# Kernel optimization log

Hardware: AMD Instinct MI355X
Metric: run time of the kernel (lower is better)

## Reference

```python
import jax, jax.numpy as jnp
import numpy as np

# Static problem constants (must match setup_inputs)
NUM_GRAPHS = 64      # batch_size = int(batch[-1]) + 1
PTS_PER_GRAPH = 512
RATIO = 16           # centroids per graph
HEADS = 4
IN_CH = 64           # = out_channels per head (concat=False -> mean over heads)
NEG_SLOPE = 0.2


def setup_inputs() -> dict:
    key = jax.random.key(0)
    ks = jax.random.split(key, 8)
    N = NUM_GRAPHS * PTS_PER_GRAPH
    x = jax.random.normal(ks[0], (N, IN_CH), dtype=jnp.float32)
    edge_index = jnp.zeros((2, 2), dtype=jnp.int64)  # unused by forward
    batch = (jnp.arange(N) // PTS_PER_GRAPH).astype(jnp.int64)
    xcent_base = jax.random.normal(ks[1], (RATIO, IN_CH), dtype=jnp.float32)
    W_l = jax.random.normal(ks[2], (IN_CH, HEADS * IN_CH), dtype=jnp.float32) / np.sqrt(IN_CH)
    b_l = jax.random.normal(ks[3], (HEADS * IN_CH,), dtype=jnp.float32) * 0.01
    W_r = jax.random.normal(ks[4], (IN_CH, HEADS * IN_CH), dtype=jnp.float32) / np.sqrt(IN_CH)
    b_r = jax.random.normal(ks[5], (HEADS * IN_CH,), dtype=jnp.float32) * 0.01
    att = jax.random.normal(ks[6], (HEADS, IN_CH), dtype=jnp.float32) / np.sqrt(IN_CH)
    bias = jax.random.normal(ks[7], (IN_CH,), dtype=jnp.float32) * 0.01
    return {"x": x, "edge_index": edge_index, "batch": batch,
            "xcent_base": xcent_base, "W_l": W_l, "b_l": b_l,
            "W_r": W_r, "b_r": b_r, "att": att, "bias": bias}


def _bipart_pool(x, batch, xcent_base, W_l, b_l, W_r, b_r, att, bias):
    N = x.shape[0]
    B = NUM_GRAPHS
    Nc = B * RATIO  # number of centroid (target) nodes

    # Dense bipartite edges: each source node -> all RATIO centroids of its graph.
    src = jnp.repeat(jnp.arange(N, dtype=jnp.int32), RATIO)                     # [E]
    dst = jnp.tile(jnp.arange(RATIO, dtype=jnp.int32), N) \
        + jnp.repeat(batch.astype(jnp.int32), RATIO) * RATIO                    # [E]

    # PyG GATv2Conv(add_self_loops=True): remove src==dst edges, then add
    # self loops (i,i) for i < min(N_src, N_dst) = Nc. Keep static shapes by
    # masking the removed edges instead of deleting them.
    self_idx = jnp.arange(Nc, dtype=jnp.int32)
    src_f = jnp.concatenate([src, self_idx])
    dst_f = jnp.concatenate([dst, self_idx])
    drop = jnp.concatenate([src == dst, jnp.zeros((Nc,), dtype=bool)])          # [E+Nc]

    # Linear projections (source and target sides)
    x_l = (x @ W_l + b_l).reshape(N, HEADS, IN_CH)                              # [N,H,C]
    xcent = jnp.tile(xcent_base, (B, 1))                                        # [Nc,IN]
    x_r = (xcent @ W_r + b_r).reshape(Nc, HEADS, IN_CH)                         # [Nc,H,C]

    # GATv2 attention: leaky_relu(x_i + x_j) . att, softmax per target node
    xj = x_l[src_f]                                                             # [E',H,C]
    g = jax.nn.leaky_relu(xj + x_r[dst_f], NEG_SLOPE)
    alpha = jnp.einsum('ehc,hc->eh', g, att)                                    # [E',H]
    alpha = jnp.where(drop[:, None], jnp.float32(-1e30), alpha)
    amax = jax.ops.segment_max(alpha, dst_f, num_segments=Nc)                   # [Nc,H]
    e = jnp.exp(alpha - amax[dst_f])
    den = jax.ops.segment_sum(e, dst_f, num_segments=Nc)                        # [Nc,H]
    w = e / den[dst_f]                                                          # [E',H]

    out = jax.ops.segment_sum(w[..., None] * xj, dst_f, num_segments=Nc)        # [Nc,H,C]
    out = out.mean(axis=1) + bias                                               # concat=False -> mean heads
    return out.reshape(B, RATIO, IN_CH)


def reference(x, edge_index, batch, xcent_base, W_l, b_l, W_r, b_r, att, bias):
    xcent = _bipart_pool(x, batch, xcent_base, W_l, b_l, W_r, b_r, att, bias)
    batchcent = jnp.repeat(jnp.arange(NUM_GRAPHS, dtype=jnp.int64), RATIO)
    return xcent, batchcent
```

## Files before the change

kernel.cpp:

```cpp
#include <hip/hip_runtime.h>

#define PTS 512
#define CH  64
#define NC  1024

using s8v = __attribute__((ext_vector_type(8))) short;
using f4v = __attribute__((ext_vector_type(4))) float;

static __device__ __forceinline__ unsigned short f2b(float f) {
    unsigned u = __float_as_uint(f);
    return (unsigned short)((u + 0x7FFFu + ((u >> 16) & 1u)) >> 16);
}
static __device__ __forceinline__ float b2f(unsigned short s) {
    return __uint_as_float((unsigned)s << 16);
}

__global__ __launch_bounds__(256) void k0(
    const float* __restrict__ xcb, const float* __restrict__ W_r,
    const float* __restrict__ b_r, const float* __restrict__ att,
    float* __restrict__ axr, float* __restrict__ sxr)
{
    __shared__ float s_row[256];
    const int h = blockIdx.x >> 2, rq = blockIdx.x & 3;
    const int rl = threadIdx.x >> 6, c = threadIdx.x & 63;
    const int r = rq * 4 + rl;
    float acc = b_r[h * 64 + c];
    for (int k = 0; k < 64; ++k)
        acc = fmaf(xcb[r * 64 + k], W_r[k * 256 + h * 64 + c], acc);
    axr[(h * 16 + r) * 64 + c] = fabsf(att[h * 64 + c]) * acc;
    s_row[rl * 64 + c] = acc;
    __syncthreads();
    if (threadIdx.x < 4) {
        float s = 0.f;
        for (int cc = 0; cc < 64; ++cc)
            s = fmaf(s_row[threadIdx.x * 64 + cc], att[h * 64 + cc], s);
        sxr[h * 16 + rq * 4 + threadIdx.x] = s;
    }
}

__global__ __launch_bounds__(256, 2) void k1(
    const float* __restrict__ x, const float* __restrict__ W_l,
    const float* __restrict__ b_l, const float* __restrict__ att,
    const float* __restrict__ axr_ws, const float* __restrict__ sxr_ws,
    const float* __restrict__ bias,
    float* __restrict__ aws, unsigned short* __restrict__ xlself,
    float* __restrict__ out)
{
    __shared__ unsigned short s_xl[64 * 264];
    __shared__ float s_axr[4096];
    __shared__ float s_patt[256], s_sgn[256];
    __shared__ float s_sxr[64];

    const int tid = threadIdx.x;
    const int lane = tid & 63;
    const int w = __builtin_amdgcn_readfirstlane(tid >> 6);
    const int blk = blockIdx.x;
    const int row0 = blk * 64;
    const int l15 = lane & 15, quad = lane >> 4;

    {
        float av = att[tid];
        s_patt[tid] = fabsf(av);
        s_sgn[tid] = av < 0.f ? -1.f : 1.f;
    }
    for (int idx = tid; idx < 4096; idx += 256) s_axr[idx] = axr_ws[idx];
    if (tid < 64) s_sxr[tid] = sxr_ws[tid];

    f4v acc[4][4];
    const f4v zf = {0.f, 0.f, 0.f, 0.f};
#pragma unroll
    for (int m = 0; m < 4; ++m)
#pragma unroll
        for (int n = 0; n < 4; ++n) acc[m][n] = zf;

#pragma unroll
    for (int ks = 0; ks < 2; ++ks) {
        s8v Af[4], Bf[4];
#pragma unroll
        for (int m = 0; m < 4; ++m) {
            const float* xp = x + (size_t)(row0 + m * 16 + l15) * 64 + ks * 32 + quad * 8;
            float4 u0 = *(const float4*)xp;
            float4 u1 = *(const float4*)(xp + 4);
            s8v a;
            a[0] = (short)f2b(u0.x); a[1] = (short)f2b(u0.y);
            a[2] = (short)f2b(u0.z); a[3] = (short)f2b(u0.w);
            a[4] = (short)f2b(u1.x); a[5] = (short)f2b(u1.y);
            a[6] = (short)f2b(u1.z); a[7] = (short)f2b(u1.w);
            Af[m] = a;
        }
#pragma unroll
        for (int n = 0; n < 4; ++n) {
            s8v bv;
#pragma unroll
            for (int j = 0; j < 8; ++j)
                bv[j] = (short)f2b(W_l[(size_t)(ks * 32 + quad * 8 + j) * 256
                                       + w * 64 + n * 16 + l15]);
            Bf[n] = bv;
        }
#pragma unroll
        for (int m = 0; m < 4; ++m)
#pragma unroll
            for (int n = 0; n < 4; ++n)
                acc[m][n] = __builtin_amdgcn_mfma_f32_16x16x32_bf16(
                    Af[m], Bf[n], acc[m][n], 0, 0, 0);
    }

    float blv[4];
#pragma unroll
    for (int n = 0; n < 4; ++n) blv[n] = b_l[w * 64 + n * 16 + l15];
#pragma unroll
    for (int m = 0; m < 4; ++m)
#pragma unroll
        for (int n = 0; n < 4; ++n) {
            int ch = w * 64 + n * 16 + l15;
#pragma unroll
            for (int qq = 0; qq < 4; ++qq) {
                int row = m * 16 + quad * 4 + qq;
                s_xl[row * 264 + ch] = f2b(acc[m][n][qq] + blv[n]);
            }
        }

    if (blk >= 16 && blk < 20) {
        int base = (blk - 16) * 16384;
        float bv = bias[tid & 63];
#pragma unroll
        for (int j = 0; j < 64; ++j) out[base + j * 256 + tid] = bv;
    }
    if (blk == 20) {
#pragma unroll
        for (int j = 0; j < 4; ++j) {
            int c = j * 256 + tid;
            out[65536 + c] = (float)(c >> 4);
        }
    }

    __syncthreads();

    if (blk < 16) {
#pragma unroll
        for (int t = 0; t < 8; ++t) {
            int idx = tid + t * 256;
            int row = idx >> 5, co = (idx & 31) * 8;
            uint4 v = *(const uint4*)&s_xl[row * 264 + co];
            *(uint4*)&xlself[(size_t)(row0 + row) * 256 + co] = v;
        }
    }

    float axl[64];
    float sxl = 0.f;
#pragma unroll
    for (int c8 = 0; c8 < 8; ++c8) {
        uint4 raw = *(const uint4*)&s_xl[lane * 264 + w * 64 + c8 * 8];
        unsigned uu[4] = {raw.x, raw.y, raw.z, raw.w};
        float v[8];
#pragma unroll
        for (int p = 0; p < 4; ++p) {
            v[2 * p]     = __uint_as_float(uu[p] << 16);
            v[2 * p + 1] = __uint_as_float(uu[p] & 0xffff0000u);
        }
#pragma unroll
        for (int t = 0; t < 8; ++t) {
            int c = c8 * 8 + t;
            float a = s_patt[w * 64 + c] * v[t];
            axl[c] = a;
            sxl = fmaf(s_sgn[w * 64 + c], a, sxl);
        }
    }

    float ac[16];
#pragma unroll
    for (int r = 0; r < 16; ++r) ac[r] = 0.f;
#pragma unroll 4
    for (int cq = 0; cq < 16; ++cq) {
        float4 sg = *(const float4*)&s_sgn[w * 64 + cq * 4];
        float x0 = axl[cq * 4 + 0], x1 = axl[cq * 4 + 1];
        float x2 = axl[cq * 4 + 2], x3 = axl[cq * 4 + 3];
#pragma unroll
        for (int r = 0; r < 16; ++r) {
            float4 ax = *(const float4*)&s_axr[w * 1024 + r * 64 + cq * 4];
            ac[r] = fmaf(sg.x, fabsf(x0 + ax.x), ac[r]);
            ac[r] = fmaf(sg.y, fabsf(x1 + ax.y), ac[r]);
            ac[r] = fmaf(sg.z, fabsf(x2 + ax.z), ac[r]);
            ac[r] = fmaf(sg.w, fabsf(x3 + ax.w), ac[r]);
        }
    }

    float* ap = aws + ((size_t)(blk >> 3) * 4 + w) * 8192 + (blk & 7) * 64 + lane;
#pragma unroll
    for (int r = 0; r < 16; ++r)
        ap[r * 512] = 0.6f * (sxl + s_sxr[w * 16 + r]) + 0.4f * ac[r];
}

__global__ __launch_bounds__(512, 1) void k2(
    const float* __restrict__ x, const float* __restrict__ W_l,
    const float* __restrict__ b_l, const float* __restrict__ aws,
    const unsigned short* __restrict__ xlself, float* __restrict__ out)
{
    __shared__ float s_et[8192];
    __shared__ float sW[4096];
    __shared__ float s_y[1024];
    __shared__ float s_m[16], s_inv[16], s_f[16];

    const int bh = blockIdx.x, b = bh >> 2, h = bh & 3;
    const int tid = threadIdx.x;
    const float* abh = aws + (size_t)bh * 8192;

    for (int idx = tid; idx < 4096; idx += 512)
        sW[idx] = W_l[(idx >> 6) * 256 + h * 64 + (idx & 63)];
    for (int idx = tid; idx < 8192; idx += 512) {
        int r = idx >> 9, i = idx & 511;
        s_et[i * 16 + r] = abh[idx];
    }

    {
        const int r = tid >> 5, lg = tid & 31;
        const int snode = b * 16 + r;
        const float a_self = aws[(size_t)((snode >> 9) * 4 + h) * 8192
                                 + r * 512 + (snode & 511)];
        float m = a_self;
        for (int j = 0; j < 16; ++j) {
            int i = lg + j * 32;
            float a = abh[r * 512 + i];
            if (b == 0 && i == r) a = -1e30f;
            m = fmaxf(m, a);
        }
#pragma unroll
        for (int off = 16; off >= 1; off >>= 1) m = fmaxf(m, __shfl_xor(m, off));
        float d = 0.f;
        for (int j = 0; j < 16; ++j) {
            int i = lg + j * 32;
            float a = abh[r * 512 + i];
            d += (b == 0 && i == r) ? 0.f : __expf(a - m);
        }
#pragma unroll
        for (int off = 16; off >= 1; off >>= 1) d += __shfl_xor(d, off);
        if (lg == 0) {
            float es = __expf(a_self - m);
            float inv = 1.f / (d + es);
            s_m[r] = m; s_inv[r] = inv; s_f[r] = es * inv;
        }
    }
    __syncthreads();

    for (int idx = tid; idx < 8192; idx += 512) {
        int i = idx >> 4, r = idx & 15;
        float a = s_et[idx];
        float e = (b == 0 && i == r) ? 0.f : __expf(a - s_m[r]) * s_inv[r];
        s_et[idx] = e;
    }
    __syncthreads();

    const int kt = tid & 15, rt = (tid >> 4) & 3, is = tid >> 6;
    float y4[4][4];
#pragma unroll
    for (int i = 0; i < 4; ++i)
#pragma unroll
        for (int j = 0; j < 4; ++j) y4[i][j] = 0.f;

    const float* xb = x + ((size_t)b * PTS + is * 64) * 64;
#pragma unroll 4
    for (int ii = 0; ii < 64; ++ii) {
        float4 xv = *(const float4*)(xb + ii * 64 + kt * 4);
        float4 ev = *(const float4*)&s_et[(is * 64 + ii) * 16 + rt * 4];
        y4[0][0] = fmaf(ev.x, xv.x, y4[0][0]); y4[0][1] = fmaf(ev.x, xv.y, y4[0][1]);
        y4[0][2] = fmaf(ev.x, xv.z, y4[0][2]); y4[0][3] = fmaf(ev.x, xv.w, y4[0][3]);
        y4[1][0] = fmaf(ev.y, xv.x, y4[1][0]); y4[1][1] = fmaf(ev.y, xv.y, y4[1][1]);
        y4[1][2] = fmaf(ev.y, xv.z, y4[1][2]); y4[1][3] = fmaf(ev.y, xv.w, y4[1][3]);
        y4[2][0] = fmaf(ev.z, xv.x, y4[2][0]); y4[2][1] = fmaf(ev.z, xv.y, y4[2][1]);
        y4[2][2] = fmaf(ev.z, xv.z, y4[2][2]); y4[2][3] = fmaf(ev.z, xv.w, y4[2][3]);
        y4[3][0] = fmaf(ev.w, xv.x, y4[3][0]); y4[3][1] = fmaf(ev.w, xv.y, y4[3][1]);
        y4[3][2] = fmaf(ev.w, xv.z, y4[3][2]); y4[3][3] = fmaf(ev.w, xv.w, y4[3][3]);
    }
    __syncthreads();

#pragma unroll
    for (int rr = 0; rr < 4; ++rr)
        *(float4*)&s_et[is * 1024 + (rt * 4 + rr) * 64 + kt * 4] =
            make_float4(y4[rr][0], y4[rr][1], y4[rr][2], y4[rr][3]);
    __syncthreads();

    for (int o = tid; o < 1024; o += 512) {
        float s = 0.f;
#pragma unroll
        for (int sl = 0; sl < 8; ++sl) s += s_et[sl * 1024 + o];
        s_y[o] = s;
    }
    __syncthreads();

    for (int o = tid; o < 1024; o += 512) {
        int r = o >> 6, ch = o & 63;
        float a = 0.f;
#pragma unroll
        for (int k = 0; k < 64; ++k)
            a = fmaf(s_y[r * 64 + k], sW[k * 64 + ch], a);
        float f = s_f[r];
        float val = a + (1.f - f) * b_l[h * 64 + ch]
                  + f * b2f(xlself[(size_t)(b * 16 + r) * 256 + h * 64 + ch]);
        atomicAdd(&out[(b * 16 + r) * 64 + ch], 0.25f * val);
    }
}

extern "C" void kernel_launch(void* const* d_in, const int* in_sizes, int n_in,
                              void* d_out, int out_size, void* d_ws, size_t ws_size,
                              hipStream_t stream) {
    (void)in_sizes; (void)n_in; (void)out_size; (void)ws_size;
    const float* x    = (const float*)d_in[0];
    const float* xcb  = (const float*)d_in[3];
    const float* W_l  = (const float*)d_in[4];
    const float* b_l  = (const float*)d_in[5];
    const float* W_r  = (const float*)d_in[6];
    const float* b_r  = (const float*)d_in[7];
    const float* att  = (const float*)d_in[8];
    const float* bias = (const float*)d_in[9];
    float* out = (float*)d_out;

    float* wsf = (float*)d_ws;
    float*          aws    = wsf;
    float*          axr_ws = wsf + 2097152;
    float*          sxr_ws = wsf + 2101248;
    unsigned short* xlself = (unsigned short*)(wsf + 2101312);

    hipLaunchKernelGGL(k0, dim3(16), dim3(256), 0, stream,
                       xcb, W_r, b_r, att, axr_ws, sxr_ws);
    hipLaunchKernelGGL(k1, dim3(512), dim3(256), 0, stream,
                       x, W_l, b_l, att, axr_ws, sxr_ws, bias, aws, xlself, out);
    hipLaunchKernelGGL(k2, dim3(256), dim3(512), 0, stream,
                       x, W_l, b_l, aws, xlself, out);
}
```

Measured before the change: 125.7 us.

## Pre-transpose W_l to bf16 in k0 and read attention inputs from global directly

k0 gains extra blocks that convert W_l into a transposed bf16 layout, so k1 loads each B fragment with one vector load instead of eight strided scalar loads plus conversions. k1 no longer stages axr, att signs and sxr in shared memory. It reads raw xr and att from global (cached), using att*|xl+xr| directly instead of the sign/abs factorisation. The attention accumulation is restructured into two 32-channel halves to reduce register pressure. The cost is more global/L2 traffic in the inner loop and one extra workspace buffer.

```diff
diff --git a/kernel.cpp b/kernel.cpp
--- a/kernel.cpp
+++ b/kernel.cpp
@@ -18,38 +18,47 @@
 __global__ __launch_bounds__(256) void k0(
     const float* __restrict__ xcb, const float* __restrict__ W_r,
     const float* __restrict__ b_r, const float* __restrict__ att,
-    float* __restrict__ axr, float* __restrict__ sxr)
+    const float* __restrict__ W_l,
+    float* __restrict__ xr_ws, float* __restrict__ sxr_ws,
+    unsigned short* __restrict__ Wt)
 {
     __shared__ float s_row[256];
-    const int h = blockIdx.x >> 2, rq = blockIdx.x & 3;
-    const int rl = threadIdx.x >> 6, c = threadIdx.x & 63;
-    const int r = rq * 4 + rl;
-    float acc = b_r[h * 64 + c];
-    for (int k = 0; k < 64; ++k)
-        acc = fmaf(xcb[r * 64 + k], W_r[k * 256 + h * 64 + c], acc);
-    axr[(h * 16 + r) * 64 + c] = fabsf(att[h * 64 + c]) * acc;
-    s_row[rl * 64 + c] = acc;
-    __syncthreads();
-    if (threadIdx.x < 4) {
-        float s = 0.f;
-        for (int cc = 0; cc < 64; ++cc)
-            s = fmaf(s_row[threadIdx.x * 64 + cc], att[h * 64 + cc], s);
-        sxr[h * 16 + rq * 4 + threadIdx.x] = s;
+    const int blk = blockIdx.x, tid = threadIdx.x;
+    if (blk < 16) {
+        const int h = blk >> 2, rq = blk & 3;
+        const int rl = tid >> 6, c = tid & 63;
+        const int r = rq * 4 + rl;
+        float acc = b_r[h * 64 + c];
+        for (int k = 0; k < 64; ++k)
+            acc = fmaf(xcb[r * 64 + k], W_r[k * 256 + h * 64 + c], acc);
+        xr_ws[(h * 16 + r) * 64 + c] = acc;
+        s_row[rl * 64 + c] = acc;
+        __syncthreads();
+        if (tid < 4) {
+            float s = 0.f;
+            for (int cc = 0; cc < 64; ++cc)
+                s = fmaf(s_row[tid * 64 + cc], att[h * 64 + cc], s);
+            sxr_ws[h * 16 + rq * 4 + tid] = s;
+        }
+    } else {
+        int base = (blk - 16) * 2048;
+        for (int t = tid; t < 2048; t += 256) {
+            int idx = base + t;
+            int h = idx >> 12, ch = (idx >> 6) & 63, k = idx & 63;
+            Wt[idx] = f2b(W_l[k * 256 + h * 64 + ch]);
+        }
     }
 }
 
 __global__ __launch_bounds__(256, 2) void k1(
-    const float* __restrict__ x, const float* __restrict__ W_l,
+    const float* __restrict__ x, const unsigned short* __restrict__ Wt,
     const float* __restrict__ b_l, const float* __restrict__ att,
-    const float* __restrict__ axr_ws, const float* __restrict__ sxr_ws,
+    const float* __restrict__ xr_ws, const float* __restrict__ sxr_ws,
     const float* __restrict__ bias,
     float* __restrict__ aws, unsigned short* __restrict__ xlself,
     float* __restrict__ out)
 {
     __shared__ unsigned short s_xl[64 * 264];
-    __shared__ float s_axr[4096];
-    __shared__ float s_patt[256], s_sgn[256];
-    __shared__ float s_sxr[64];
 
     const int tid = threadIdx.x;
     const int lane = tid & 63;
@@ -57,14 +66,6 @@
     const int blk = blockIdx.x;
     const int row0 = blk * 64;
     const int l15 = lane & 15, quad = lane >> 4;
-
-    {
-        float av = att[tid];
-        s_patt[tid] = fabsf(av);
-        s_sgn[tid] = av < 0.f ? -1.f : 1.f;
-    }
-    for (int idx = tid; idx < 4096; idx += 256) s_axr[idx] = axr_ws[idx];
-    if (tid < 64) s_sxr[tid] = sxr_ws[tid];
 
     f4v acc[4][4];
     const f4v zf = {0.f, 0.f, 0.f, 0.f};
@@ -89,14 +90,9 @@
             Af[m] = a;
         }
 #pragma unroll
-        for (int n = 0; n < 4; ++n) {
-            s8v bv;
-#pragma unroll
-            for (int j = 0; j < 8; ++j)
-                bv[j] = (short)f2b(W_l[(size_t)(ks * 32 + quad * 8 + j) * 256
-                                       + w * 64 + n * 16 + l15]);
-            Bf[n] = bv;
-        }
+        for (int n = 0; n < 4; ++n)
+            Bf[n] = *(const s8v*)(Wt + (size_t)(w * 64 + n * 16 + l15) * 64
+                                  + ks * 32 + quad * 8);
 #pragma unroll
         for (int m = 0; m < 4; ++m)
 #pragma unroll
@@ -146,49 +142,56 @@
         }
     }
 
-    float axl[64];
+    const float* attw = att + w * 64;
+    const float* xrw  = xr_ws + w * 1024;
+    float ac[16];
+#pragma unroll
+    for (int r = 0; r < 16; ++r) ac[r] = 0.f;
     float sxl = 0.f;
-#pragma unroll
-    for (int c8 = 0; c8 < 8; ++c8) {
-        uint4 raw = *(const uint4*)&s_xl[lane * 264 + w * 64 + c8 * 8];
-        unsigned uu[4] = {raw.x, raw.y, raw.z, raw.w};
-        float v[8];
-#pragma unroll
-        for (int p = 0; p < 4; ++p) {
-            v[2 * p]     = __uint_as_float(uu[p] << 16);
-            v[2 * p + 1] = __uint_as_float(uu[p] & 0xffff0000u);
-        }
-#pragma unroll
-        for (int t = 0; t < 8; ++t) {
-            int c = c8 * 8 + t;
-            float a = s_patt[w * 64 + c] * v[t];
-            axl[c] = a;
-            sxl = fmaf(s_sgn[w * 64 + c], a, sxl);
-        }
-    }
-
-    float ac[16];
-#pragma unroll
-    for (int r = 0; r < 16; ++r) ac[r] = 0.f;
-#pragma unroll 4
-    for (int cq = 0; cq < 16; ++cq) {
-        float4 sg = *(const float4*)&s_sgn[w * 64 + cq * 4];
-        float x0 = axl[cq * 4 + 0], x1 = axl[cq * 4 + 1];
-        float x2 = axl[cq * 4 + 2], x3 = axl[cq * 4 + 3];
-#pragma unroll
+
+#pragma unroll
+    for (int half = 0; half < 2; ++half) {
+        const int cb = half * 32;
+        float xlv[32], atv[32];
+#pragma unroll
+        for (int c8 = 0; c8 < 4; ++c8) {
+            uint4 raw = *(const uint4*)&s_xl[lane * 264 + w * 64 + cb + c8 * 8];
+            unsigned uu[4] = {raw.x, raw.y, raw.z, raw.w};
+#pragma unroll
+            for (int p = 0; p < 4; ++p) {
+                xlv[c8 * 8 + 2 * p]     = __uint_as_float(uu[p] << 16);
+                xlv[c8 * 8 + 2 * p + 1] = __uint_as_float(uu[p] & 0xffff0000u);
+            }
+        }
+#pragma unroll
+        for (int cq = 0; cq < 8; ++cq) {
+            float4 a4 = *(const float4*)(attw + cb + cq * 4);
+            atv[cq * 4 + 0] = a4.x; atv[cq * 4 + 1] = a4.y;
+            atv[cq * 4 + 2] = a4.z; atv[cq * 4 + 3] = a4.w;
+        }
+#pragma unroll
+        for (int t = 0; t < 32; ++t) sxl = fmaf(atv[t], xlv[t], sxl);
+
+#pragma unroll 2
         for (int r = 0; r < 16; ++r) {
-            float4 ax = *(const float4*)&s_axr[w * 1024 + r * 64 + cq * 4];
-            ac[r] = fmaf(sg.x, fabsf(x0 + ax.x), ac[r]);
-            ac[r] = fmaf(sg.y, fabsf(x1 + ax.y), ac[r]);
-            ac[r] = fmaf(sg.z, fabsf(x2 + ax.z), ac[r]);
-            ac[r] = fmaf(sg.w, fabsf(x3 + ax.w), ac[r]);
+            const float4* xrp = (const float4*)(xrw + r * 64 + cb);
+            float a = 0.f;
+#pragma unroll
+            for (int cq = 0; cq < 8; ++cq) {
+                float4 x4 = xrp[cq];
+                a = fmaf(atv[cq * 4 + 0], fabsf(xlv[cq * 4 + 0] + x4.x), a);
+                a = fmaf(atv[cq * 4 + 1], fabsf(xlv[cq * 4 + 1] + x4.y), a);
+                a = fmaf(atv[cq * 4 + 2], fabsf(xlv[cq * 4 + 2] + x4.z), a);
+                a = fmaf(atv[cq * 4 + 3], fabsf(xlv[cq * 4 + 3] + x4.w), a);
+            }
+            ac[r] += a;
         }
     }
 
     float* ap = aws + ((size_t)(blk >> 3) * 4 + w) * 8192 + (blk & 7) * 64 + lane;
 #pragma unroll
     for (int r = 0; r < 16; ++r)
-        ap[r * 512] = 0.6f * (sxl + s_sxr[w * 16 + r]) + 0.4f * ac[r];
+        ap[r * 512] = 0.6f * (sxl + sxr_ws[w * 16 + r]) + 0.4f * ac[r];
 }
 
 __global__ __launch_bounds__(512, 1) void k2(
@@ -316,14 +319,15 @@
 
     float* wsf = (float*)d_ws;
     float*          aws    = wsf;
-    float*          axr_ws = wsf + 2097152;
+    float*          xr_ws  = wsf + 2097152;
     float*          sxr_ws = wsf + 2101248;
-    unsigned short* xlself = (unsigned short*)(wsf + 2101312);
-
-    hipLaunchKernelGGL(k0, dim3(16), dim3(256), 0, stream,
-                       xcb, W_r, b_r, att, axr_ws, sxr_ws);
+    unsigned short* Wt     = (unsigned short*)(wsf + 2101376);
+    unsigned short* xlself = (unsigned short*)(wsf + 2109568);
+
+    hipLaunchKernelGGL(k0, dim3(24), dim3(256), 0, stream,
+                       xcb, W_r, b_r, att, W_l, xr_ws, sxr_ws, Wt);
     hipLaunchKernelGGL(k1, dim3(512), dim3(256), 0, stream,
-                       x, W_l, b_l, att, axr_ws, sxr_ws, bias, aws, xlself, out);
+                       x, Wt, b_l, att, xr_ws, sxr_ws, bias, aws, xlself, out);
     hipLaunchKernelGGL(k2, dim3(256), dim3(512), 0, stream,
                        x, W_l, b_l, aws, xlself, out);
 }
```

Result: faster. 119.3 us (-5.2%).
